# Optimization experiments

Measured on AMD Instinct MI355X. Metric: run time of the kernel, lower is better.

Reference implementation:

```python
import jax, jax.numpy as jnp
import numpy as np

B, C, T = 16, 2048, 128      # batch, enc_in (variables), d_model
ID, NC, CD, GD, OUT = 32, 16, 32, 32, 96  # id_dim, num_clusters, cluster_dim, graph_dim, out_len
GIN = T + ID + CD            # gcn_input_dim = 192
NEG = -1.0e9


def setup_inputs() -> dict:
    key = jax.random.key(0)
    ks = jax.random.split(key, 13)
    s = 0.02
    return {
        "x": jax.random.normal(ks[0], (B, C, 1, T), dtype=jnp.float32),
        "id_emb": jax.random.normal(ks[1], (C, ID), dtype=jnp.float32) * s,
        "w1": jax.random.normal(ks[2], (T, T // 2), dtype=jnp.float32) * s,
        "b1": jnp.zeros((T // 2,), dtype=jnp.float32),
        "w2": jax.random.normal(ks[3], (T // 2, ID), dtype=jnp.float32) * s,
        "b2": jnp.zeros((ID,), dtype=jnp.float32),
        "cluster_emb": jax.random.normal(ks[4], (NC, CD), dtype=jnp.float32) * s,
        "wic": jax.random.normal(ks[5], (ID, CD), dtype=jnp.float32) * s,
        "bic": jnp.zeros((CD,), dtype=jnp.float32),
        "wg": jax.random.normal(ks[6], (ID + CD, GD), dtype=jnp.float32) * s,
        "bg": jnp.zeros((GD,), dtype=jnp.float32),
        "context_weight": jax.random.normal(ks[7], (C, GIN), dtype=jnp.float32) * s,
        "wl": jax.random.normal(ks[8], (GIN, OUT), dtype=jnp.float32) * s,
        "bl": jnp.zeros((OUT,), dtype=jnp.float32),
    }


def reference(x, id_emb, w1, b1, w2, b2, cluster_emb, wic, bic, wg, bg,
              context_weight, wl, bl):
    b, c, n, t = x.shape
    xs = x[:, :, 0, :]                                       # [b,c,t] (squeeze dim -2)
    # dynamic id projection: Linear -> ReLU -> Linear
    dyn = jax.nn.relu(xs @ w1 + b1) @ w2 + b2                # [b,c,id]
    id_embeds = id_emb[None, :, :] + dyn                     # static + dynamic
    # soft cluster assignment
    id_for_clustering = id_embeds @ wic + bic                # [b,c,cd]
    probs = jax.nn.softmax(
        jnp.einsum('bcl,nl->bcn', id_for_clustering, cluster_emb), axis=-1)
    cluster_embeds = probs @ cluster_emb                     # [b,c,cd]
    # graph embedding and dynamic dense adjacency
    graph_emb = jnp.concatenate([id_embeds, cluster_embeds], axis=-1) @ wg + bg
    adj = jnp.einsum('bcg,bmg->bcm', graph_emb, graph_emb)   # [b,c,c]
    adj = jax.nn.relu(adj)
    neg = NEG * jnp.eye(c, dtype=adj.dtype)                  # [c,c], -1e9 on diag, 0 off-diag
    adj = adj + neg
    # torch.where(adj<=0, neg_inf_matrix, adj): off-diag nonpositive -> 0, diag -> -1e9
    adj = jnp.where(adj <= 0.0, neg, adj)
    adj = jax.nn.softmax(adj, axis=-1)
    # two-stage GCN aggregation (dropout is identity in eval mode)
    gcn_input = jnp.concatenate([xs, id_embeds, cluster_embeds], axis=-1)  # [b,c,GIN]
    agg = jnp.einsum('boi,bid->bod', adj, gcn_input)         # [b,c,GIN]
    w = jnp.tanh(jnp.einsum('bod,ol->bdl', agg, context_weight))  # [b,GIN,GIN]
    out = (jnp.einsum('bdl,bod->bol', w, gcn_input) + gcn_input) @ wl + bl  # [b,c,out_len]
    return out[:, :, None, :]                                # unsqueeze dim -2
```

## Files before the change

kernel.cpp:

```cpp
#include <hip/hip_runtime.h>
#include <hip/hip_bf16.h>


typedef __attribute__((ext_vector_type(8))) short short8;
typedef __attribute__((ext_vector_type(16))) float f32x16;

__device__ __forceinline__ unsigned short f2bf(float f) {
    __hip_bfloat16 h = __float2bfloat16(f);
    return *reinterpret_cast<unsigned short*>(&h);
}
__device__ __forceinline__ float bf2f(unsigned short u) {
    __hip_bfloat16 h = *reinterpret_cast<__hip_bfloat16*>(&u);
    return __bfloat162float(h);
}

__global__ __launch_bounds__(256) void k0_transpose_x(
    const float* __restrict__ x, unsigned short* __restrict__ vt)
{
    __shared__ float sT[64 * 133];
    const int t = threadIdx.x;
    const int m0 = blockIdx.x * 64;
    const int b = blockIdx.y;
    const float* xb = x + (size_t)b * 2048 * 128;
    #pragma unroll
    for (int kk = 0; kk < 8; ++kk) {
        int i = t + kk * 256;
        int mm = i >> 5, q4 = i & 31;
        float4 v = ((const float4*)(xb + (size_t)(m0 + mm) * 128))[q4];
        float* d = sT + mm * 133 + q4 * 4;
        d[0] = v.x; d[1] = v.y; d[2] = v.z; d[3] = v.w;
    }
    __syncthreads();
    const int mp = t & 31;
    const int ch0 = t >> 5;
    #pragma unroll
    for (int pass = 0; pass < 16; ++pass) {
        int ch = ch0 + pass * 8;
        unsigned int u0 = f2bf(sT[(2 * mp) * 133 + ch]);
        unsigned int u1 = f2bf(sT[(2 * mp + 1) * 133 + ch]);
        *((unsigned int*)(vt + (size_t)(b * 192 + ch) * 2048 + m0) + mp) =
            u0 | (u1 << 16);
    }
}

__global__ __launch_bounds__(256) void k1_tiled(
    const float* __restrict__ x, const float* __restrict__ id_emb,
    const float* __restrict__ w1, const float* __restrict__ b1,
    const float* __restrict__ w2, const float* __restrict__ b2,
    const float* __restrict__ ce, const float* __restrict__ wic,
    const float* __restrict__ bic, const float* __restrict__ wg,
    const float* __restrict__ bg, unsigned short* __restrict__ vt,
    unsigned short* __restrict__ geb16)
{
    __shared__ float sxs[32 * 132];
    __shared__ float sh[32 * 68];
    __shared__ float sid[32 * 36];
    __shared__ float sic[32 * 36];
    __shared__ float scl[32 * 36];
    __shared__ float sp[32 * 20];

    const int t = threadIdx.x;
    const int r0 = blockIdx.x * 32;
    const int b = r0 >> 11;
    const int c0 = r0 & 2047;

    #pragma unroll
    for (int p = 0; p < 4; ++p) {
        int i4 = t + p * 256;
        int row = i4 >> 5, q = i4 & 31;
        float4 v = ((const float4*)(x + (size_t)r0 * 128))[i4];
        *(float4*)(sxs + row * 132 + q * 4) = v;
    }
    __syncthreads();

    {
        const int row = t >> 3, j0 = (t & 7) * 8;
        const float* xr = sxs + row * 132;
        float acc[8];
        #pragma unroll
        for (int j = 0; j < 8; ++j) acc[j] = b1[j0 + j];
        float4 pa[4], pb[4];
        float  px[4];
        #pragma unroll
        for (int u = 0; u < 4; ++u) {
            const float4* wr = (const float4*)(w1 + u * 64 + j0);
            pa[u] = wr[0]; pb[u] = wr[1]; px[u] = xr[u];
        }
        for (int k0 = 0; k0 < 128; k0 += 4) {
            float4 ca[4], cb[4];
            float  cx[4];
            #pragma unroll
            for (int u = 0; u < 4; ++u) { ca[u] = pa[u]; cb[u] = pb[u]; cx[u] = px[u]; }
            const int kn = k0 + 4;
            if (kn < 128) {
                #pragma unroll
                for (int u = 0; u < 4; ++u) {
                    const float4* wr = (const float4*)(w1 + (kn + u) * 64 + j0);
                    pa[u] = wr[0]; pb[u] = wr[1]; px[u] = xr[kn + u];
                }
            }
            #pragma unroll
            for (int u = 0; u < 4; ++u) {
                acc[0] = fmaf(cx[u], ca[u].x, acc[0]);
                acc[1] = fmaf(cx[u], ca[u].y, acc[1]);
                acc[2] = fmaf(cx[u], ca[u].z, acc[2]);
                acc[3] = fmaf(cx[u], ca[u].w, acc[3]);
                acc[4] = fmaf(cx[u], cb[u].x, acc[4]);
                acc[5] = fmaf(cx[u], cb[u].y, acc[5]);
                acc[6] = fmaf(cx[u], cb[u].z, acc[6]);
                acc[7] = fmaf(cx[u], cb[u].w, acc[7]);
            }
        }
        float* hr = sh + row * 68 + j0;
        #pragma unroll
        for (int j = 0; j < 8; ++j) hr[j] = fmaxf(acc[j], 0.f);
    }
    __syncthreads();

    {
        const int row = t >> 3, j0 = (t & 7) * 4;
        const int c = c0 + row;
        const float* hrow = sh + row * 68;
        float acc[4];
        #pragma unroll
        for (int j = 0; j < 4; ++j) acc[j] = b2[j0 + j];
        float4 pw[4];
        float  ph[4];
        #pragma unroll
        for (int u = 0; u < 4; ++u) {
            pw[u] = *(const float4*)(w2 + u * 32 + j0);
            ph[u] = hrow[u];
        }
        for (int k0 = 0; k0 < 64; k0 += 4) {
            float4 cw4[4];
            float  ch4[4];
            #pragma unroll
            for (int u = 0; u < 4; ++u) { cw4[u] = pw[u]; ch4[u] = ph[u]; }
            const int kn = k0 + 4;
            if (kn < 64) {
                #pragma unroll
                for (int u = 0; u < 4; ++u) {
                    pw[u] = *(const float4*)(w2 + (kn + u) * 32 + j0);
                    ph[u] = hrow[kn + u];
                }
            }
            #pragma unroll
            for (int u = 0; u < 4; ++u) {
                acc[0] = fmaf(ch4[u], cw4[u].x, acc[0]);
                acc[1] = fmaf(ch4[u], cw4[u].y, acc[1]);
                acc[2] = fmaf(ch4[u], cw4[u].z, acc[2]);
                acc[3] = fmaf(ch4[u], cw4[u].w, acc[3]);
            }
        }
        #pragma unroll
        for (int j = 0; j < 4; ++j) {
            float ide = id_emb[c * 32 + j0 + j] + acc[j];
            sid[row * 36 + j0 + j] = ide;
            vt[(size_t)(b * 192 + 128 + j0 + j) * 2048 + c] = f2bf(ide);
        }
    }
    __syncthreads();

    {
        const int row = t >> 3, j0 = (t & 7) * 4;
        const float* irow = sid + row * 36;
        float acc[4];
        #pragma unroll
        for (int j = 0; j < 4; ++j) acc[j] = bic[j0 + j];
        float4 pw[4];
        float  pi[4];
        #pragma unroll
        for (int u = 0; u < 4; ++u) {
            pw[u] = *(const float4*)(wic + u * 32 + j0);
            pi[u] = irow[u];
        }
        for (int k0 = 0; k0 < 32; k0 += 4) {
            float4 cw4[4];
            float  ci4[4];
            #pragma unroll
            for (int u = 0; u < 4; ++u) { cw4[u] = pw[u]; ci4[u] = pi[u]; }
            const int kn = k0 + 4;
            if (kn < 32) {
                #pragma unroll
                for (int u = 0; u < 4; ++u) {
                    pw[u] = *(const float4*)(wic + (kn + u) * 32 + j0);
                    pi[u] = irow[kn + u];
                }
            }
            #pragma unroll
            for (int u = 0; u < 4; ++u) {
                acc[0] = fmaf(ci4[u], cw4[u].x, acc[0]);
                acc[1] = fmaf(ci4[u], cw4[u].y, acc[1]);
                acc[2] = fmaf(ci4[u], cw4[u].z, acc[2]);
                acc[3] = fmaf(ci4[u], cw4[u].w, acc[3]);
            }
        }
        #pragma unroll
        for (int j = 0; j < 4; ++j) sic[row * 36 + j0 + j] = acc[j];
    }
    __syncthreads();

    {
        const int n = t & 15, rowp = t >> 4;
        const float* cer = ce + n * 32;
        float a0 = 0.f, a1 = 0.f;
        #pragma unroll
        for (int k0 = 0; k0 < 32; k0 += 8) {
            float cv[8], s0[8], s1[8];
            #pragma unroll
            for (int u = 0; u < 8; ++u) {
                cv[u] = cer[k0 + u];
                s0[u] = sic[rowp * 36 + k0 + u];
                s1[u] = sic[(rowp + 16) * 36 + k0 + u];
            }
            #pragma unroll
            for (int u = 0; u < 8; ++u) {
                a0 = fmaf(s0[u], cv[u], a0);
                a1 = fmaf(s1[u], cv[u], a1);
            }
        }
        sp[rowp * 20 + n] = a0;
        sp[(rowp + 16) * 20 + n] = a1;
    }
    __syncthreads();

    if (t < 32) {
        float* pr = sp + t * 20;
        float mx = pr[0];
        for (int n = 1; n < 16; ++n) mx = fmaxf(mx, pr[n]);
        float ss = 0.f;
        for (int n = 0; n < 16; ++n) { float e = __expf(pr[n] - mx); pr[n] = e; ss += e; }
        float inv = 1.f / ss;
        for (int n = 0; n < 16; ++n) pr[n] *= inv;
    }
    __syncthreads();

    {
        const int row = t >> 3, j0 = (t & 7) * 4;
        const int c = c0 + row;
        const float* prow = sp + row * 20;
        float acc[4] = {0.f, 0.f, 0.f, 0.f};
        float4 pc[4];
        float  pp[4];
        #pragma unroll
        for (int u = 0; u < 4; ++u) {
            pc[u] = *(const float4*)(ce + u * 32 + j0);
            pp[u] = prow[u];
        }
        for (int n0 = 0; n0 < 16; n0 += 4) {
            float4 cc4[4];
            float  cp4[4];
            #pragma unroll
            for (int u = 0; u < 4; ++u) { cc4[u] = pc[u]; cp4[u] = pp[u]; }
            const int nn = n0 + 4;
            if (nn < 16) {
                #pragma unroll
                for (int u = 0; u < 4; ++u) {
                    pc[u] = *(const float4*)(ce + (nn + u) * 32 + j0);
                    pp[u] = prow[nn + u];
                }
            }
            #pragma unroll
            for (int u = 0; u < 4; ++u) {
                acc[0] = fmaf(cp4[u], cc4[u].x, acc[0]);
                acc[1] = fmaf(cp4[u], cc4[u].y, acc[1]);
                acc[2] = fmaf(cp4[u], cc4[u].z, acc[2]);
                acc[3] = fmaf(cp4[u], cc4[u].w, acc[3]);
            }
        }
        #pragma unroll
        for (int j = 0; j < 4; ++j) {
            scl[row * 36 + j0 + j] = acc[j];
            vt[(size_t)(b * 192 + 160 + j0 + j) * 2048 + c] = f2bf(acc[j]);
        }
    }
    __syncthreads();

    {
        const int row = t >> 3, j0 = (t & 7) * 4;
        const int r = r0 + row;
        const float* irow = sid + row * 36;
        const float* crow = scl + row * 36;
        float acc[4];
        #pragma unroll
        for (int j = 0; j < 4; ++j) acc[j] = bg[j0 + j];
        {
            float4 pw[4];
            float  pi[4];
            #pragma unroll
            for (int u = 0; u < 4; ++u) {
                pw[u] = *(const float4*)(wg + u * 32 + j0);
                pi[u] = irow[u];
            }
            for (int k0 = 0; k0 < 32; k0 += 4) {
                float4 cw4[4];
                float  ci4[4];
                #pragma unroll
                for (int u = 0; u < 4; ++u) { cw4[u] = pw[u]; ci4[u] = pi[u]; }
                const int kn = k0 + 4;
                if (kn < 32) {
                    #pragma unroll
                    for (int u = 0; u < 4; ++u) {
                        pw[u] = *(const float4*)(wg + (kn + u) * 32 + j0);
                        pi[u] = irow[kn + u];
                    }
                }
                #pragma unroll
                for (int u = 0; u < 4; ++u) {
                    acc[0] = fmaf(ci4[u], cw4[u].x, acc[0]);
                    acc[1] = fmaf(ci4[u], cw4[u].y, acc[1]);
                    acc[2] = fmaf(ci4[u], cw4[u].z, acc[2]);
                    acc[3] = fmaf(ci4[u], cw4[u].w, acc[3]);
                }
            }
        }
        {
            float4 pw[4];
            float  pcv[4];
            #pragma unroll
            for (int u = 0; u < 4; ++u) {
                pw[u] = *(const float4*)(wg + (32 + u) * 32 + j0);
                pcv[u] = crow[u];
            }
            for (int k0 = 0; k0 < 32; k0 += 4) {
                float4 cw4[4];
                float  cc4[4];
                #pragma unroll
                for (int u = 0; u < 4; ++u) { cw4[u] = pw[u]; cc4[u] = pcv[u]; }
                const int kn = k0 + 4;
                if (kn < 32) {
                    #pragma unroll
                    for (int u = 0; u < 4; ++u) {
                        pw[u] = *(const float4*)(wg + (32 + kn + u) * 32 + j0);
                        pcv[u] = crow[kn + u];
                    }
                }
                #pragma unroll
                for (int u = 0; u < 4; ++u) {
                    acc[0] = fmaf(cc4[u], cw4[u].x, acc[0]);
                    acc[1] = fmaf(cc4[u], cw4[u].y, acc[1]);
                    acc[2] = fmaf(cc4[u], cw4[u].z, acc[2]);
                    acc[3] = fmaf(cc4[u], cw4[u].w, acc[3]);
                }
            }
        }
        #pragma unroll
        for (int j = 0; j < 4; ++j)
            geb16[(size_t)r * 32 + j0 + j] = f2bf(acc[j]);
    }
}

__global__ __launch_bounds__(256) void k1b_sumv(
    const unsigned short* __restrict__ vt, float* __restrict__ sumv)
{
    __shared__ float red[256];
    const int ch = blockIdx.x, b = blockIdx.y, t = threadIdx.x;
    const unsigned short* row = vt + (size_t)(b * 192 + ch) * 2048;
    float a = 0.f;
    #pragma unroll
    for (int j = 0; j < 8; ++j) a += bf2f(row[t * 8 + j]);
    red[t] = a; __syncthreads();
    for (int off = 128; off > 0; off >>= 1) {
        if (t < off) red[t] += red[t + off];
        __syncthreads();
    }
    if (t == 0) sumv[b * 192 + ch] = red[0];
}

__global__ __launch_bounds__(256) void k2_fused(
    const unsigned short* __restrict__ geb16,
    const unsigned short* __restrict__ vt,
    const float* __restrict__ sumv,
    unsigned short* __restrict__ aggb)
{
    __shared__ unsigned short sGeO[64 * 40];
    __shared__ unsigned short sGe[2][64 * 40];
    __shared__ unsigned short sVtA[2][192 * 72];
    __shared__ unsigned short dw[64 * 72];
    __shared__ float s_sum[192];
    __shared__ float sinv[64];
    float* lpbuf = (float*)sVtA;

    const int t = threadIdx.x;
    const int b = blockIdx.y;
    const int o0 = blockIdx.x * 64;
    const unsigned short* geb = geb16 + (size_t)b * 2048 * 32;
    const unsigned short* vtb = vt + (size_t)b * 192 * 2048;

    const int lane = t & 63;
    const int mg = t >> 6;
    const int col = lane & 31;
    const int grp = lane >> 5;
    const int os = (mg & 1) * 32;
    const int ms = (mg >> 1) * 32;
    const int orow0 = (mg & 1) * 32;
    const int dbase = (mg >> 1) * 96;

    const int ge_row = t >> 2, ge_c8 = t & 3;

    short8 rGe;
    short8 rVt0, rVt1, rVt2, rVt3, rVt4, rVt5;

    if (t < 192) s_sum[t] = sumv[b * 192 + t];
    {
        short8 v = *(const short8*)(geb + (size_t)(o0 + ge_row) * 32 + ge_c8 * 8);
        *(short8*)(sGeO + ge_row * 40 + ge_c8 * 8) = v;
    }
    {
        rGe = *(const short8*)(geb + (size_t)ge_row * 32 + ge_c8 * 8);
        int i0;
        i0 = t + 0 * 256; rVt0 = *(const short8*)(vtb + (size_t)(i0 >> 3) * 2048 + 0 + (i0 & 7) * 8);
        i0 = t + 1 * 256; rVt1 = *(const short8*)(vtb + (size_t)(i0 >> 3) * 2048 + 0 + (i0 & 7) * 8);
        i0 = t + 2 * 256; rVt2 = *(const short8*)(vtb + (size_t)(i0 >> 3) * 2048 + 0 + (i0 & 7) * 8);
        i0 = t + 3 * 256; rVt3 = *(const short8*)(vtb + (size_t)(i0 >> 3) * 2048 + 0 + (i0 & 7) * 8);
        i0 = t + 4 * 256; rVt4 = *(const short8*)(vtb + (size_t)(i0 >> 3) * 2048 + 0 + (i0 & 7) * 8);
        i0 = t + 5 * 256; rVt5 = *(const short8*)(vtb + (size_t)(i0 >> 3) * 2048 + 0 + (i0 & 7) * 8);
    }
    {
        *(short8*)(sGe[0] + ge_row * 40 + ge_c8 * 8) = rGe;
        int i0;
        i0 = t + 0 * 256; *(short8*)(sVtA[0] + (i0 >> 3) * 72 + (i0 & 7) * 8) = rVt0;
        i0 = t + 1 * 256; *(short8*)(sVtA[0] + (i0 >> 3) * 72 + (i0 & 7) * 8) = rVt1;
        i0 = t + 2 * 256; *(short8*)(sVtA[0] + (i0 >> 3) * 72 + (i0 & 7) * 8) = rVt2;
        i0 = t + 3 * 256; *(short8*)(sVtA[0] + (i0 >> 3) * 72 + (i0 & 7) * 8) = rVt3;
        i0 = t + 4 * 256; *(short8*)(sVtA[0] + (i0 >> 3) * 72 + (i0 & 7) * 8) = rVt4;
        i0 = t + 5 * 256; *(short8*)(sVtA[0] + (i0 >> 3) * 72 + (i0 & 7) * 8) = rVt5;
    }
    __syncthreads();

    f32x16 acc0, acc1, acc2;
    #pragma unroll
    for (int i = 0; i < 16; ++i) { acc0[i] = 0.f; acc1[i] = 0.f; acc2[i] = 0.f; }
    float lpA[16];
    #pragma unroll
    for (int i = 0; i < 16; ++i) lpA[i] = 0.f;

    int cur = 0;
    for (int m0 = 0; m0 < 2048; m0 += 64) {
        const bool have_next = (m0 + 64 < 2048);

        if (have_next) {
            const int mn = m0 + 64;
            rGe = *(const short8*)(geb + (size_t)(mn + ge_row) * 32 + ge_c8 * 8);
            int i0;
            i0 = t + 0 * 256; rVt0 = *(const short8*)(vtb + (size_t)(i0 >> 3) * 2048 + mn + (i0 & 7) * 8);
            i0 = t + 1 * 256; rVt1 = *(const short8*)(vtb + (size_t)(i0 >> 3) * 2048 + mn + (i0 & 7) * 8);
            i0 = t + 2 * 256; rVt2 = *(const short8*)(vtb + (size_t)(i0 >> 3) * 2048 + mn + (i0 & 7) * 8);
            i0 = t + 3 * 256; rVt3 = *(const short8*)(vtb + (size_t)(i0 >> 3) * 2048 + mn + (i0 & 7) * 8);
            i0 = t + 4 * 256; rVt4 = *(const short8*)(vtb + (size_t)(i0 >> 3) * 2048 + mn + (i0 & 7) * 8);
            i0 = t + 5 * 256; rVt5 = *(const short8*)(vtb + (size_t)(i0 >> 3) * 2048 + mn + (i0 & 7) * 8);
        }

        f32x16 sacc;
        #pragma unroll
        for (int i = 0; i < 16; ++i) sacc[i] = 0.f;
        #pragma unroll
        for (int ks = 0; ks < 2; ++ks) {
            short8 A  = *(const short8*)(sGeO + (os + col) * 40 + ks * 16 + grp * 8);
            short8 Bf = *(const short8*)(sGe[cur] + (ms + col) * 40 + ks * 16 + grp * 8);
            sacc = __builtin_amdgcn_mfma_f32_32x32x16_bf16(A, Bf, sacc, 0, 0, 0);
        }
        {
            const int m_local = ms + col;
            const int gm = m0 + m_local;
            #pragma unroll
            for (int r = 0; r < 16; ++r) {
                int o_local = os + (r & 3) + 8 * (r >> 2) + 4 * grp;
                float s = sacc[r];
                float d = (gm == o0 + o_local) ? -1.f
                        : ((s > 0.f) ? (__expf(s) - 1.f) : 0.f);
                lpA[r] += d;
                dw[o_local * 72 + m_local] = f2bf(d);
            }
        }
        __syncthreads();

        #pragma unroll
        for (int ks = 0; ks < 4; ++ks) {
            short8 A  = *(const short8*)(dw + (orow0 + col) * 72 + ks * 16 + grp * 8);
            short8 B0 = *(const short8*)(sVtA[cur] + (dbase + col) * 72 + ks * 16 + grp * 8);
            short8 B1 = *(const short8*)(sVtA[cur] + (dbase + 32 + col) * 72 + ks * 16 + grp * 8);
            short8 B2 = *(const short8*)(sVtA[cur] + (dbase + 64 + col) * 72 + ks * 16 + grp * 8);
            acc0 = __builtin_amdgcn_mfma_f32_32x32x16_bf16(A, B0, acc0, 0, 0, 0);
            acc1 = __builtin_amdgcn_mfma_f32_32x32x16_bf16(A, B1, acc1, 0, 0, 0);
            acc2 = __builtin_amdgcn_mfma_f32_32x32x16_bf16(A, B2, acc2, 0, 0, 0);
        }

        if (have_next) {
            const int nb = cur ^ 1;
            *(short8*)(sGe[nb] + ge_row * 40 + ge_c8 * 8) = rGe;
            int i0;
            i0 = t + 0 * 256; *(short8*)(sVtA[nb] + (i0 >> 3) * 72 + (i0 & 7) * 8) = rVt0;
            i0 = t + 1 * 256; *(short8*)(sVtA[nb] + (i0 >> 3) * 72 + (i0 & 7) * 8) = rVt1;
            i0 = t + 2 * 256; *(short8*)(sVtA[nb] + (i0 >> 3) * 72 + (i0 & 7) * 8) = rVt2;
            i0 = t + 3 * 256; *(short8*)(sVtA[nb] + (i0 >> 3) * 72 + (i0 & 7) * 8) = rVt3;
            i0 = t + 4 * 256; *(short8*)(sVtA[nb] + (i0 >> 3) * 72 + (i0 & 7) * 8) = rVt4;
            i0 = t + 5 * 256; *(short8*)(sVtA[nb] + (i0 >> 3) * 72 + (i0 & 7) * 8) = rVt5;
        }
        __syncthreads();
        cur ^= 1;
    }

    {
        const int widx = mg >> 1;
        #pragma unroll
        for (int r = 0; r < 16; ++r) {
            int ol = os + (r & 3) + 8 * (r >> 2) + 4 * grp;
            lpbuf[(widx * 32 + col) * 68 + ol] = lpA[r];
        }
    }
    __syncthreads();
    if (t < 64) {
        float l = 2048.f;
        for (int i = 0; i < 64; ++i) l += lpbuf[i * 68 + t];
        sinv[t] = 1.f / l;
    }
    __syncthreads();

    {
        f32x16 av[3] = {acc0, acc1, acc2};
        unsigned short* ab = aggb + (size_t)b * 2048 * 192;
        #pragma unroll
        for (int n = 0; n < 3; ++n) {
            int chn = dbase + n * 32 + col;
            float sv = s_sum[chn];
            #pragma unroll
            for (int r = 0; r < 16; ++r) {
                int ol = orow0 + (r & 3) + 8 * (r >> 2) + 4 * grp;
                ab[(size_t)(o0 + ol) * 192 + chn] =
                    f2bf((sv + av[n][r]) * sinv[ol]);
            }
        }
    }
}

__global__ __launch_bounds__(256) void k3_ctx_sk(
    const unsigned short* __restrict__ aggb, const float* __restrict__ cw,
    float* __restrict__ wpart)
{
    __shared__ float sA[64 * 68];
    __shared__ float sW[64 * 68];
    const int t = threadIdx.x;
    const int slot = blockIdx.z;
    const int b = slot >> 3;
    const int ks = slot & 7;
    const int d0 = blockIdx.x * 64;
    const int l0 = blockIdx.y * 64;
    const unsigned short* ab = aggb + (size_t)b * 2048 * 192;
    const int ti = t >> 4, tj = t & 15;
    float acc[4][4] = {{0.f}};

    for (int o0 = ks * 256; o0 < ks * 256 + 256; o0 += 64) {
        for (int i = t; i < 4096; i += 256) {
            int oo = i >> 6, dd = i & 63;
            sA[oo * 68 + dd] = bf2f(ab[(size_t)(o0 + oo) * 192 + d0 + dd]);
            sW[oo * 68 + dd] = cw[(size_t)(o0 + oo) * 192 + l0 + dd];
        }
        __syncthreads();
        for (int o = 0; o < 64; ++o) {
            const float* ap = sA + o * 68 + ti * 4;
            const float* wp = sW + o * 68 + tj * 4;
            float a0 = ap[0], a1 = ap[1], a2 = ap[2], a3 = ap[3];
            float w0 = wp[0], w1v = wp[1], w2v = wp[2], w3 = wp[3];
            acc[0][0] = fmaf(a0, w0, acc[0][0]); acc[0][1] = fmaf(a0, w1v, acc[0][1]);
            acc[0][2] = fmaf(a0, w2v, acc[0][2]); acc[0][3] = fmaf(a0, w3, acc[0][3]);
            acc[1][0] = fmaf(a1, w0, acc[1][0]); acc[1][1] = fmaf(a1, w1v, acc[1][1]);
            acc[1][2] = fmaf(a1, w2v, acc[1][2]); acc[1][3] = fmaf(a1, w3, acc[1][3]);
            acc[2][0] = fmaf(a2, w0, acc[2][0]); acc[2][1] = fmaf(a2, w1v, acc[2][1]);
            acc[2][2] = fmaf(a2, w2v, acc[2][2]); acc[2][3] = fmaf(a2, w3, acc[2][3]);
            acc[3][0] = fmaf(a3, w0, acc[3][0]); acc[3][1] = fmaf(a3, w1v, acc[3][1]);
            acc[3][2] = fmaf(a3, w2v, acc[3][2]); acc[3][3] = fmaf(a3, w3, acc[3][3]);
        }
        __syncthreads();
    }
    float* wp = wpart + (size_t)slot * 36864;
    #pragma unroll
    for (int i = 0; i < 4; ++i)
        #pragma unroll
        for (int j = 0; j < 4; ++j)
            wp[(d0 + ti * 4 + i) * 192 + l0 + tj * 4 + j] = acc[i][j];
}

__global__ __launch_bounds__(256) void k3r_reduce(
    const float* __restrict__ wpart, float* __restrict__ wraw)
{
    const int idx = blockIdx.x * 256 + threadIdx.x;
    const int b = blockIdx.y;
    const float* base = wpart + (size_t)b * 8 * 36864 + idx;
    float a = 0.f;
    #pragma unroll
    for (int ks = 0; ks < 8; ++ks) a += base[(size_t)ks * 36864];
    wraw[(size_t)b * 36864 + idx] = tanhf(a);
}

__global__ __launch_bounds__(256) void k3_ctx(
    const unsigned short* __restrict__ aggb, const float* __restrict__ cw,
    float* __restrict__ wraw)
{
    __shared__ float sA[64 * 68];
    __shared__ float sW[64 * 68];
    const int t = threadIdx.x;
    const int b = blockIdx.z;
    const int d0 = blockIdx.x * 64;
    const int l0 = blockIdx.y * 64;
    const unsigned short* ab = aggb + (size_t)b * 2048 * 192;
    const int ti = t >> 4, tj = t & 15;
    float acc[4][4] = {{0.f}};

    for (int o0 = 0; o0 < 2048; o0 += 64) {
        for (int i = t; i < 4096; i += 256) {
            int oo = i >> 6, dd = i & 63;
            sA[oo * 68 + dd] = bf2f(ab[(size_t)(o0 + oo) * 192 + d0 + dd]);
            sW[oo * 68 + dd] = cw[(size_t)(o0 + oo) * 192 + l0 + dd];
        }
        __syncthreads();
        for (int o = 0; o < 64; ++o) {
            const float* ap = sA + o * 68 + ti * 4;
            const float* wp = sW + o * 68 + tj * 4;
            float a0 = ap[0], a1 = ap[1], a2 = ap[2], a3 = ap[3];
            float w0 = wp[0], w1v = wp[1], w2v = wp[2], w3 = wp[3];
            acc[0][0] = fmaf(a0, w0, acc[0][0]); acc[0][1] = fmaf(a0, w1v, acc[0][1]);
            acc[0][2] = fmaf(a0, w2v, acc[0][2]); acc[0][3] = fmaf(a0, w3, acc[0][3]);
            acc[1][0] = fmaf(a1, w0, acc[1][0]); acc[1][1] = fmaf(a1, w1v, acc[1][1]);
            acc[1][2] = fmaf(a1, w2v, acc[1][2]); acc[1][3] = fmaf(a1, w3, acc[1][3]);
            acc[2][0] = fmaf(a2, w0, acc[2][0]); acc[2][1] = fmaf(a2, w1v, acc[2][1]);
            acc[2][2] = fmaf(a2, w2v, acc[2][2]); acc[2][3] = fmaf(a2, w3, acc[2][3]);
            acc[3][0] = fmaf(a3, w0, acc[3][0]); acc[3][1] = fmaf(a3, w1v, acc[3][1]);
            acc[3][2] = fmaf(a3, w2v, acc[3][2]); acc[3][3] = fmaf(a3, w3, acc[3][3]);
        }
        __syncthreads();
    }
    float* wb = wraw + (size_t)b * 36864;
    #pragma unroll
    for (int i = 0; i < 4; ++i)
        #pragma unroll
        for (int j = 0; j < 4; ++j)
            wb[(d0 + ti * 4 + i) * 192 + l0 + tj * 4 + j] = tanhf(acc[i][j]);
}

__global__ __launch_bounds__(192) void k3b_m2(
    const float* __restrict__ wmat, const float* __restrict__ wl,
    float* __restrict__ m2)
{
    const int t = threadIdx.x;
    const int b = blockIdx.y;
    const int d = blockIdx.x * 2 + (t / 96);
    const int l = t % 96;
    const float* wrow = wmat + (size_t)b * 36864 + d * 192;
    float acc = wl[d * 96 + l];
    for (int k = 0; k < 192; ++k)
        acc = fmaf(wrow[k], wl[k * 96 + l], acc);
    m2[(size_t)b * 18432 + d * 96 + l] = acc;
}

__global__ __launch_bounds__(192) void k4_tiled(
    const float* __restrict__ x, const unsigned short* __restrict__ vt,
    const float* __restrict__ m2, const float* __restrict__ bl,
    float* __restrict__ out)
{
    __shared__ float sm2[192 * 96];
    const int t = threadIdx.x;
    const int rblk = blockIdx.x;
    const int b = blockIdx.y;
    {
        const float4* src = (const float4*)(m2 + (size_t)b * 18432);
        float4* dst = (float4*)sm2;
        #pragma unroll
        for (int i = 0; i < 24; ++i) dst[t + i * 192] = src[t + i * 192];
    }
    __syncthreads();

    const int rg = t / 12;
    const int cg = t % 12;
    const int j0 = cg * 8;
    const int cloc = rblk * 64 + rg * 4;
    const int rr = b * 2048 + cloc;
    float acc[4][8];
    #pragma unroll
    for (int i = 0; i < 4; ++i)
        #pragma unroll
        for (int j = 0; j < 8; ++j) acc[i][j] = bl[j0 + j];

    for (int k0 = 0; k0 < 128; k0 += 8) {
        float rv[4][8];
        #pragma unroll
        for (int i = 0; i < 4; ++i) {
            const float4* xr = (const float4*)(x + (size_t)(rr + i) * 128 + k0);
            float4 a = xr[0], c4 = xr[1];
            rv[i][0] = a.x; rv[i][1] = a.y; rv[i][2] = a.z; rv[i][3] = a.w;
            rv[i][4] = c4.x; rv[i][5] = c4.y; rv[i][6] = c4.z; rv[i][7] = c4.w;
        }
        #pragma unroll
        for (int kk = 0; kk < 8; ++kk) {
            const float* mr = sm2 + (k0 + kk) * 96 + j0;
            float mv[8];
            #pragma unroll
            for (int j = 0; j < 8; ++j) mv[j] = mr[j];
            #pragma unroll
            for (int i = 0; i < 4; ++i)
                #pragma unroll
                for (int j = 0; j < 8; ++j)
                    acc[i][j] = fmaf(rv[i][kk], mv[j], acc[i][j]);
        }
    }
    for (int k = 128; k < 192; ++k) {
        const unsigned short* vr = vt + (size_t)(b * 192 + k) * 2048 + cloc;
        float rv0 = bf2f(vr[0]), rv1 = bf2f(vr[1]);
        float rv2 = bf2f(vr[2]), rv3 = bf2f(vr[3]);
        const float* mr = sm2 + k * 96 + j0;
        #pragma unroll
        for (int j = 0; j < 8; ++j) {
            float mv = mr[j];
            acc[0][j] = fmaf(rv0, mv, acc[0][j]);
            acc[1][j] = fmaf(rv1, mv, acc[1][j]);
            acc[2][j] = fmaf(rv2, mv, acc[2][j]);
            acc[3][j] = fmaf(rv3, mv, acc[3][j]);
        }
    }
    #pragma unroll
    for (int i = 0; i < 4; ++i) {
        float* orow = out + (size_t)(rr + i) * 96 + j0;
        *(float4*)orow = make_float4(acc[i][0], acc[i][1], acc[i][2], acc[i][3]);
        *(float4*)(orow + 4) = make_float4(acc[i][4], acc[i][5], acc[i][6], acc[i][7]);
    }
}

extern "C" void kernel_launch(void* const* d_in, const int* in_sizes, int n_in,
                              void* d_out, int out_size, void* d_ws, size_t ws_size,
                              hipStream_t stream) {
    const float* x      = (const float*)d_in[0];
    const float* id_emb = (const float*)d_in[1];
    const float* w1     = (const float*)d_in[2];
    const float* b1     = (const float*)d_in[3];
    const float* w2     = (const float*)d_in[4];
    const float* b2     = (const float*)d_in[5];
    const float* ce     = (const float*)d_in[6];
    const float* wic    = (const float*)d_in[7];
    const float* bic    = (const float*)d_in[8];
    const float* wg     = (const float*)d_in[9];
    const float* bg     = (const float*)d_in[10];
    const float* cw     = (const float*)d_in[11];
    const float* wl     = (const float*)d_in[12];
    const float* bl     = (const float*)d_in[13];
    float* out = (float*)d_out;

    float* ws = (float*)d_ws;
    unsigned short* vt    = (unsigned short*)ws;
    unsigned short* geb16 = (unsigned short*)(ws + 3145728);
    unsigned short* aggb  = (unsigned short*)(ws + 3670016);
    float* wraw  = ws + 6815744;
    float* m2    = ws + 7405568;
    float* sumv  = ws + 7700480;
    float* wpart = ws + 7703552;
    const size_t need_sk = (7703552ull + 4718592ull) * 4ull;
    const bool use_sk = (ws_size >= need_sk);

    hipLaunchKernelGGL(k0_transpose_x, dim3(32, 16), dim3(256), 0, stream, x, vt);
    hipLaunchKernelGGL(k1_tiled, dim3(1024), dim3(256), 0, stream,
                       x, id_emb, w1, b1, w2, b2, ce, wic, bic, wg, bg, vt, geb16);
    hipLaunchKernelGGL(k1b_sumv, dim3(192, 16), dim3(256), 0, stream, vt, sumv);
    hipLaunchKernelGGL(k2_fused, dim3(32, 16), dim3(256), 0, stream,
                       geb16, vt, sumv, aggb);
    if (use_sk) {
        hipLaunchKernelGGL(k3_ctx_sk, dim3(3, 3, 128), dim3(256), 0, stream,
                           aggb, cw, wpart);
        hipLaunchKernelGGL(k3r_reduce, dim3(144, 16), dim3(256), 0, stream,
                           wpart, wraw);
    } else {
        hipLaunchKernelGGL(k3_ctx, dim3(3, 3, 16), dim3(256), 0, stream,
                           aggb, cw, wraw);
    }
    hipLaunchKernelGGL(k3b_m2, dim3(96, 16), dim3(192), 0, stream,
                       wraw, wl, m2);
    hipLaunchKernelGGL(k4_tiled, dim3(32, 16), dim3(192), 0, stream,
                       x, vt, m2, bl, out);
}
```

Measured before the change: 300.3 us.

## Swizzle LDS tiles, remap block order per XCD, split diagonal branch in k2

```diff
diff --git a/kernel.cpp b/kernel.cpp
--- a/kernel.cpp
+++ b/kernel.cpp
@@ -12,6 +12,9 @@
 __device__ __forceinline__ float bf2f(unsigned short u) {
     __hip_bfloat16 h = *reinterpret_cast<__hip_bfloat16*>(&u);
     return __bfloat162float(h);
+}
+__device__ __forceinline__ int swz8(int row, int off16) {
+    return off16 ^ (((row >> 3) & 3) << 3);
 }
 
 __global__ __launch_bounds__(256) void k0_transpose_x(
@@ -382,8 +385,10 @@
     float* lpbuf = (float*)sVtA;
 
     const int t = threadIdx.x;
-    const int b = blockIdx.y;
-    const int o0 = blockIdx.x * 64;
+    const int lin = blockIdx.x + gridDim.x * blockIdx.y;
+    const int nb = (lin & 7) * 64 + (lin >> 3);
+    const int o0 = (nb & 31) * 64;
+    const int b = nb >> 5;
     const unsigned short* geb = geb16 + (size_t)b * 2048 * 32;
     const unsigned short* vtb = vt + (size_t)b * 192 * 2048;
 
@@ -404,7 +409,7 @@
     if (t < 192) s_sum[t] = sumv[b * 192 + t];
     {
         short8 v = *(const short8*)(geb + (size_t)(o0 + ge_row) * 32 + ge_c8 * 8);
-        *(short8*)(sGeO + ge_row * 40 + ge_c8 * 8) = v;
+        *(short8*)(sGeO + ge_row * 40 + swz8(ge_row, ge_c8 * 8)) = v;
     }
     {
         rGe = *(const short8*)(geb + (size_t)ge_row * 32 + ge_c8 * 8);
@@ -417,14 +422,14 @@
         i0 = t + 5 * 256; rVt5 = *(const short8*)(vtb + (size_t)(i0 >> 3) * 2048 + 0 + (i0 & 7) * 8);
     }
     {
-        *(short8*)(sGe[0] + ge_row * 40 + ge_c8 * 8) = rGe;
-        int i0;
-        i0 = t + 0 * 256; *(short8*)(sVtA[0] + (i0 >> 3) * 72 + (i0 & 7) * 8) = rVt0;
-        i0 = t + 1 * 256; *(short8*)(sVtA[0] + (i0 >> 3) * 72 + (i0 & 7) * 8) = rVt1;
-        i0 = t + 2 * 256; *(short8*)(sVtA[0] + (i0 >> 3) * 72 + (i0 & 7) * 8) = rVt2;
-        i0 = t + 3 * 256; *(short8*)(sVtA[0] + (i0 >> 3) * 72 + (i0 & 7) * 8) = rVt3;
-        i0 = t + 4 * 256; *(short8*)(sVtA[0] + (i0 >> 3) * 72 + (i0 & 7) * 8) = rVt4;
-        i0 = t + 5 * 256; *(short8*)(sVtA[0] + (i0 >> 3) * 72 + (i0 & 7) * 8) = rVt5;
+        *(short8*)(sGe[0] + ge_row * 40 + swz8(ge_row, ge_c8 * 8)) = rGe;
+        int i0, ch;
+        i0 = t + 0 * 256; ch = i0 >> 3; *(short8*)(sVtA[0] + ch * 72 + swz8(ch, (i0 & 7) * 8)) = rVt0;
+        i0 = t + 1 * 256; ch = i0 >> 3; *(short8*)(sVtA[0] + ch * 72 + swz8(ch, (i0 & 7) * 8)) = rVt1;
+        i0 = t + 2 * 256; ch = i0 >> 3; *(short8*)(sVtA[0] + ch * 72 + swz8(ch, (i0 & 7) * 8)) = rVt2;
+        i0 = t + 3 * 256; ch = i0 >> 3; *(short8*)(sVtA[0] + ch * 72 + swz8(ch, (i0 & 7) * 8)) = rVt3;
+        i0 = t + 4 * 256; ch = i0 >> 3; *(short8*)(sVtA[0] + ch * 72 + swz8(ch, (i0 & 7) * 8)) = rVt4;
+        i0 = t + 5 * 256; ch = i0 >> 3; *(short8*)(sVtA[0] + ch * 72 + swz8(ch, (i0 & 7) * 8)) = rVt5;
     }
     __syncthreads();
 
@@ -456,46 +461,60 @@
         for (int i = 0; i < 16; ++i) sacc[i] = 0.f;
         #pragma unroll
         for (int ks = 0; ks < 2; ++ks) {
-            short8 A  = *(const short8*)(sGeO + (os + col) * 40 + ks * 16 + grp * 8);
-            short8 Bf = *(const short8*)(sGe[cur] + (ms + col) * 40 + ks * 16 + grp * 8);
+            int ra = os + col, rb = ms + col;
+            short8 A  = *(const short8*)(sGeO + ra * 40 + swz8(ra, ks * 16 + grp * 8));
+            short8 Bf = *(const short8*)(sGe[cur] + rb * 40 + swz8(rb, ks * 16 + grp * 8));
             sacc = __builtin_amdgcn_mfma_f32_32x32x16_bf16(A, Bf, sacc, 0, 0, 0);
         }
         {
             const int m_local = ms + col;
-            const int gm = m0 + m_local;
-            #pragma unroll
-            for (int r = 0; r < 16; ++r) {
-                int o_local = os + (r & 3) + 8 * (r >> 2) + 4 * grp;
-                float s = sacc[r];
-                float d = (gm == o0 + o_local) ? -1.f
-                        : ((s > 0.f) ? (__expf(s) - 1.f) : 0.f);
-                lpA[r] += d;
-                dw[o_local * 72 + m_local] = f2bf(d);
+            if (m0 != o0) {
+                #pragma unroll
+                for (int r = 0; r < 16; ++r) {
+                    int o_local = os + (r & 3) + 8 * (r >> 2) + 4 * grp;
+                    float s = sacc[r];
+                    float d = (s > 0.f) ? (__expf(s) - 1.f) : 0.f;
+                    lpA[r] += d;
+                    dw[o_local * 72 + swz8(o_local, m_local)] = f2bf(d);
+                }
+            } else {
+                const int gm = m0 + m_local;
+                #pragma unroll
+                for (int r = 0; r < 16; ++r) {
+                    int o_local = os + (r & 3) + 8 * (r >> 2) + 4 * grp;
+                    float s = sacc[r];
+                    float d = (gm == o0 + o_local) ? -1.f
+                            : ((s > 0.f) ? (__expf(s) - 1.f) : 0.f);
+                    lpA[r] += d;
+                    dw[o_local * 72 + swz8(o_local, m_local)] = f2bf(d);
+                }
             }
         }
         __syncthreads();
 
         #pragma unroll
         for (int ks = 0; ks < 4; ++ks) {
-            short8 A  = *(const short8*)(dw + (orow0 + col) * 72 + ks * 16 + grp * 8);
-            short8 B0 = *(const short8*)(sVtA[cur] + (dbase + col) * 72 + ks * 16 + grp * 8);
-            short8 B1 = *(const short8*)(sVtA[cur] + (dbase + 32 + col) * 72 + ks * 16 + grp * 8);
-            short8 B2 = *(const short8*)(sVtA[cur] + (dbase + 64 + col) * 72 + ks * 16 + grp * 8);
+            int rd = orow0 + col;
+            int r0c = dbase + col, r1c = dbase + 32 + col, r2c = dbase + 64 + col;
+            short8 A  = *(const short8*)(dw + rd * 72 + swz8(rd, ks * 16 + grp * 8));
+            short8 B0 = *(const short8*)(sVtA[cur] + r0c * 72 + swz8(r0c, ks * 16 + grp * 8));
+            short8 B1 = *(const short8*)(sVtA[cur] + r1c * 72 + swz8(r1c, ks * 16 + grp * 8));
+            short8 B2 = *(const short8*)(sVtA[cur] + r2c * 72 + swz8(r2c, ks * 16 + grp * 8));
             acc0 = __builtin_amdgcn_mfma_f32_32x32x16_bf16(A, B0, acc0, 0, 0, 0);
             acc1 = __builtin_amdgcn_mfma_f32_32x32x16_bf16(A, B1, acc1, 0, 0, 0);
             acc2 = __builtin_amdgcn_mfma_f32_32x32x16_bf16(A, B2, acc2, 0, 0, 0);
         }
 
         if (have_next) {
-            const int nb = cur ^ 1;
-            *(short8*)(sGe[nb] + ge_row * 40 + ge_c8 * 8) = rGe;
-            int i0;
-            i0 = t + 0 * 256; *(short8*)(sVtA[nb] + (i0 >> 3) * 72 + (i0 & 7) * 8) = rVt0;
-            i0 = t + 1 * 256; *(short8*)(sVtA[nb] + (i0 >> 3) * 72 + (i0 & 7) * 8) = rVt1;
-            i0 = t + 2 * 256; *(short8*)(sVtA[nb] + (i0 >> 3) * 72 + (i0 & 7) * 8) = rVt2;
-            i0 = t + 3 * 256; *(short8*)(sVtA[nb] + (i0 >> 3) * 72 + (i0 & 7) * 8) = rVt3;
-            i0 = t + 4 * 256; *(short8*)(sVtA[nb] + (i0 >> 3) * 72 + (i0 & 7) * 8) = rVt4;
-            i0 = t + 5 * 256; *(short8*)(sVtA[nb] + (i0 >> 3) * 72 + (i0 & 7) * 8) = rVt5;
+            const int nbuf = cur ^ 1;
+            *(short8*)(sGe[nbuf] + ge_row * 40 + swz8(ge_row, ge_c8 * 8)) = rGe;
+            int i0, ch;
+            i0 = t + 0 * 256; ch = i0 >> 3; *(short8*)(sVtA[nbuf] + ch * 72 + swz8(ch, (i0 & 7) * 8)) = rVt0;
+            i0 = t + 1 * 256; ch = i0 >> 3; *(short8*)(sVtA[nbuf] + ch * 72 + swz8(ch, (i0 & 7) * 8)) = rVt1;
+            i0 = t + 2 * 256; ch = i0 >> 3; *(short8*)(sVtA[nbuf] + ch * 72 + swz8(ch, (i0 & 7) * 8)) = rVt2;
+            i0 = t + 3 * 256; ch = i0 >> 3; *(short8*)(sVtA[nbuf] + ch * 72 + swz8(ch, (i0 & 7) * 8)) = rVt3;
+            i0 = t + 4 * 256; ch = i0 >> 3; *(short8*)(sVtA[nbuf] + ch * 72 + swz8(ch, (i0 & 7) * 8)) = rVt4;
+            i0 = t + 5 * 256; ch = i0 >> 3; *(short8*)(sVtA[nbuf] + ch * 72 + swz8(ch, (i0 & 7) * 8)) = rVt5;
         }
         __syncthreads();
         cur ^= 1;
```

Result: faster. 293.5 us (-2.3%).
